# Performance work log

Hardware: AMD Instinct MI355X
Metric: run time of the kernel (lower is better)

The kernel has to match this reference:

```python
import jax, jax.numpy as jnp
import numpy as np

H = 8
LN_EPS = 1e-5

def setup_inputs() -> dict:
    key = jax.random.key(0)
    k1, k2, k3, k4 = jax.random.split(key, 4)
    bh, q_len, dk = 64, 1024, 64
    return {
        "query": jax.random.normal(k1, (bh, q_len, dk), dtype=jnp.float32),
        "key": jax.random.normal(k2, (bh, q_len, dk), dtype=jnp.float32),
        "value": jax.random.normal(k3, (bh, q_len, dk), dtype=jnp.float32),
        "head_att": jax.random.normal(k4, (H, H), dtype=jnp.float32),
        "ln_w": jnp.ones((H,), dtype=jnp.float32),
        "ln_b": jnp.zeros((H,), dtype=jnp.float32),
    }

def reference(query, key, value, head_att, ln_w, ln_b):
    bh, q_len, dk = query.shape
    k_len = key.shape[1]
    # scores: (bh, q, k)
    scores = jnp.einsum("bqd,bkd->bqk", query, key) / jnp.sqrt(jnp.asarray(dk, query.dtype))
    attn = jax.nn.softmax(scores, axis=-1)
    # view as (B, H, q, k) then move heads last: (B, q, k, H)
    a = attn.reshape(-1, H, q_len, k_len).transpose(0, 2, 3, 1)
    # DeepViT re-attention: cross-head mixing matmul
    a = a @ head_att  # (B, q, k, H)
    # LayerNorm over head dim
    mu = a.mean(axis=-1, keepdims=True)
    var = ((a - mu) ** 2).mean(axis=-1, keepdims=True)
    a = (a - mu) * jax.lax.rsqrt(var + LN_EPS) * ln_w + ln_b
    # back to (B, H, q, k)
    a = a.transpose(0, 3, 1, 2)
    att_map = a.mean(axis=1)  # (B, q, k)
    attention = a.reshape(bh, q_len, k_len)
    out = jnp.einsum("bqk,bkd->bqd", attention, value)
    return (out, att_map)
```

## Files before the change

kernel.cpp:

```cpp
#include <hip/hip_runtime.h>
#include <hip/hip_bf16.h>

typedef _Float16 f16;
typedef f16 f16x8 __attribute__((ext_vector_type(8)));
typedef f16 f16x4 __attribute__((ext_vector_type(4)));
typedef float f32x4 __attribute__((ext_vector_type(4)));

#define QL 1024
#define KL 1024
#define DKD 64
#define NH 8
#define LNEPS 1e-5f

__global__ __launch_bounds__(256) void prep_cvt(const float* __restrict__ src,
                                                f16* __restrict__ dst, float scale) {
  int i = (blockIdx.x * 256 + threadIdx.x) * 4;
  float4 v = *reinterpret_cast<const float4*>(src + i);
  f16x4 o;
  o[0] = (f16)(v.x * scale); o[1] = (f16)(v.y * scale);
  o[2] = (f16)(v.z * scale); o[3] = (f16)(v.w * scale);
  *reinterpret_cast<f16x4*>(dst + i) = o;
}

__global__ __launch_bounds__(256) void prep_vt(const float* __restrict__ V, f16* __restrict__ vt) {
  __shared__ float t[32][33];
  const int bh = blockIdx.z, k0 = blockIdx.x * 32, d0 = blockIdx.y * 32;
  const float* src = V + ((size_t)bh * KL + k0) * DKD + d0;
#pragma unroll
  for (int j = 0; j < 4; ++j) {
    int kk = threadIdx.y * 4 + j;
    t[kk][threadIdx.x] = src[kk * DKD + threadIdx.x];
  }
  __syncthreads();
  f16* dst = vt + ((size_t)bh * DKD + d0) * KL + k0;
#pragma unroll
  for (int j = 0; j < 4; ++j) {
    int dd = threadIdx.y * 4 + j;
    dst[dd * KL + threadIdx.x] = (f16)t[threadIdx.x][dd];
  }
}

__global__ __launch_bounds__(256) void stats_kernel(const f16* __restrict__ qf,
    const f16* __restrict__ kf, float* __restrict__ rowsum) {
  const int tid = threadIdx.x;
  const int lane = tid & 63, w = tid >> 6;
  const int m = lane & 15, g = lane >> 4;
  const int id = blockIdx.x;
  const int bh = (id & 7) * 8 + ((id >> 3) & 7);
  const int q0 = (id >> 6) * 64 + w * 16;

  f16x8 qv[2];
#pragma unroll
  for (int dc = 0; dc < 2; ++dc)
    qv[dc] = *reinterpret_cast<const f16x8*>(
        qf + ((size_t)bh * QL + q0 + m) * DKD + dc * 32 + g * 8);

  float part[4] = {0.f, 0.f, 0.f, 0.f};
#pragma unroll 2
  for (int kt = 0; kt < 64; ++kt) {
    const f16* kb = kf + ((size_t)bh * KL + kt * 16 + m) * DKD + g * 8;
    f16x8 k0f = *reinterpret_cast<const f16x8*>(kb);
    f16x8 k1f = *reinterpret_cast<const f16x8*>(kb + 32);
    f32x4 acc = {0.f, 0.f, 0.f, 0.f};
    acc = __builtin_amdgcn_mfma_f32_16x16x32_f16(qv[0], k0f, acc, 0, 0, 0);
    acc = __builtin_amdgcn_mfma_f32_16x16x32_f16(qv[1], k1f, acc, 0, 0, 0);
#pragma unroll
    for (int ri = 0; ri < 4; ++ri) part[ri] += __expf(acc[ri]);
  }
#pragma unroll
  for (int ri = 0; ri < 4; ++ri) {
    float v = part[ri];
    v += __shfl_xor(v, 1); v += __shfl_xor(v, 2);
    v += __shfl_xor(v, 4); v += __shfl_xor(v, 8);
    part[ri] = v;
  }
  if (m == 0) {
#pragma unroll
    for (int ri = 0; ri < 4; ++ri) rowsum[(size_t)bh * QL + q0 + g * 4 + ri] = part[ri];
  }
}

__global__ __launch_bounds__(256) void main_kernel(
    const f16* __restrict__ qf, const f16* __restrict__ kf, const f16* __restrict__ vt,
    const float* __restrict__ rowsum,
    const float* __restrict__ hA, const float* __restrict__ lnw, const float* __restrict__ lnb,
    float* __restrict__ outp, float* __restrict__ part1, float* __restrict__ att_map) {
  __shared__ __align__(16) f16 y_lds[2][NH][16][64];

  const int tid = threadIdx.x;
  const int lane = tid & 63, w = tid >> 6;
  const int m = lane & 15, g = lane >> 4;
  const int id = blockIdx.x;
  const int b = id & 7, kc = (id >> 3) & 1, q0 = (id >> 4) * 16;

  float haR[64], wR[8], bR[8];
#pragma unroll
  for (int j = 0; j < 64; ++j) haR[j] = hA[j];
#pragma unroll
  for (int j = 0; j < 8; ++j) { wR[j] = lnw[j]; bR[j] = lnb[j]; }

  f16x8 qv[NH][2];
#pragma unroll
  for (int h = 0; h < NH; ++h)
#pragma unroll
    for (int dc = 0; dc < 2; ++dc)
      qv[h][dc] = *reinterpret_cast<const f16x8*>(
          qf + (((size_t)(b * NH + h)) * QL + q0 + m) * DKD + dc * 32 + g * 8);

  float inv_rs[NH][4];
#pragma unroll
  for (int h = 0; h < NH; ++h)
#pragma unroll
    for (int ri = 0; ri < 4; ++ri)
      inv_rs[h][ri] = 1.0f / rowsum[(size_t)(b * NH + h) * QL + q0 + g * 4 + ri];

  const size_t kbase_b = (size_t)b * NH * KL;
  f32x4 oacc[2][4];
#pragma unroll
  for (int hp = 0; hp < 2; ++hp)
#pragma unroll
    for (int dt = 0; dt < 4; ++dt) oacc[hp][dt] = (f32x4){0.f, 0.f, 0.f, 0.f};

  for (int kt = 0; kt < 8; ++kt) {
    const int kbase = kc * 512 + kt * 64;
    const int kcol = kbase + w * 16;
    const int buf = kt & 1;

    f32x4 pacc[NH];
    {
      const f16* kb = kf + (kbase_b + kcol + m) * DKD + g * 8;
#pragma unroll
      for (int h = 0; h < NH; ++h) {
        f16x8 k0f = *reinterpret_cast<const f16x8*>(kb + (size_t)h * KL * DKD);
        f16x8 k1f = *reinterpret_cast<const f16x8*>(kb + (size_t)h * KL * DKD + 32);
        f32x4 acc = {0.f, 0.f, 0.f, 0.f};
        acc = __builtin_amdgcn_mfma_f32_16x16x32_f16(qv[h][0], k0f, acc, 0, 0, 0);
        acc = __builtin_amdgcn_mfma_f32_16x16x32_f16(qv[h][1], k1f, acc, 0, 0, 0);
        pacc[h] = acc;
      }
    }
#pragma unroll
    for (int h = 0; h < NH; ++h)
#pragma unroll
      for (int ri = 0; ri < 4; ++ri)
        pacc[h][ri] = __expf(pacc[h][ri]) * inv_rs[h][ri];

#pragma unroll
    for (int ri = 0; ri < 4; ++ri) {
      const int qq = g * 4 + ri;
      float mixed[8];
      float mu = 0.f;
#pragma unroll
      for (int hh = 0; hh < 8; ++hh) {
        float s = 0.f;
#pragma unroll
        for (int j = 0; j < 8; ++j) s = fmaf(pacc[j][ri], haR[j * 8 + hh], s);
        mixed[hh] = s; mu += s;
      }
      mu *= 0.125f;
      float var = 0.f;
#pragma unroll
      for (int hh = 0; hh < 8; ++hh) { float d = mixed[hh] - mu; var = fmaf(d, d, var); }
      var *= 0.125f;
      const float rsv = rsqrtf(var + LNEPS);
      float am = 0.f;
      const int kidx = ((((2 * w + (m >> 3)) ^ (qq & 7)) << 3) | (m & 7));
#pragma unroll
      for (int hh = 0; hh < 8; ++hh) {
        float y = (mixed[hh] - mu) * rsv * wR[hh] + bR[hh];
        am += y;
        y_lds[buf][hh][qq][kidx] = (f16)y;
      }
      att_map[((size_t)b * QL + q0 + qq) * KL + kcol + m] = am * 0.125f;
    }
    __syncthreads();

#pragma unroll
    for (int hp = 0; hp < 2; ++hp) {
      const int hh = w + hp * 4;
      const f16* vb = vt + (((size_t)(b * NH + hh)) * DKD + m) * KL + kbase + g * 8;
#pragma unroll
      for (int ks = 0; ks < 2; ++ks) {
        const f16x8 af = *reinterpret_cast<const f16x8*>(
            &y_lds[buf][hh][m][((ks * 4 + g) ^ (m & 7)) << 3]);
#pragma unroll
        for (int dt = 0; dt < 4; ++dt) {
          f16x8 vf = *reinterpret_cast<const f16x8*>(vb + (size_t)dt * 16 * KL + ks * 32);
          oacc[hp][dt] = __builtin_amdgcn_mfma_f32_16x16x32_f16(af, vf, oacc[hp][dt], 0, 0, 0);
        }
      }
    }
  }

  float* dst = kc ? part1 : outp;
#pragma unroll
  for (int hp = 0; hp < 2; ++hp) {
    const int hh = w + hp * 4;
#pragma unroll
    for (int dt = 0; dt < 4; ++dt)
#pragma unroll
      for (int ri = 0; ri < 4; ++ri)
        dst[(((size_t)(b * NH + hh)) * QL + q0 + g * 4 + ri) * DKD + dt * 16 + m] =
            oacc[hp][dt][ri];
  }
}

__global__ __launch_bounds__(256) void reduce_kernel(const float* __restrict__ p1,
                                                     float* __restrict__ outp) {
  size_t i = ((size_t)blockIdx.x * 256 + threadIdx.x) * 4;
  float4 a = *reinterpret_cast<const float4*>(outp + i);
  float4 c = *reinterpret_cast<const float4*>(p1 + i);
  a.x += c.x; a.y += c.y; a.z += c.z; a.w += c.w;
  *reinterpret_cast<float4*>(outp + i) = a;
}

extern "C" void kernel_launch(void* const* d_in, const int* in_sizes, int n_in,
                              void* d_out, int out_size, void* d_ws, size_t ws_size,
                              hipStream_t stream) {
  const float* Qm  = (const float*)d_in[0];
  const float* Km  = (const float*)d_in[1];
  const float* Vm  = (const float*)d_in[2];
  const float* hA  = (const float*)d_in[3];
  const float* lnw = (const float*)d_in[4];
  const float* lnb = (const float*)d_in[5];
  float* outp = (float*)d_out;
  float* att_map = outp + (size_t)64 * QL * DKD;

  char* ws = (char*)d_ws;
  f16* kfp   = (f16*)ws;
  f16* vtp   = (f16*)(ws + (size_t)8388608);
  f16* qfp   = (f16*)(ws + (size_t)16777216);
  float* rsm = (float*)(ws + (size_t)25165824);
  float* p1  = (float*)(ws + (size_t)25427968);

  prep_cvt<<<4096, 256, 0, stream>>>(Km, kfp, 1.0f);
  prep_cvt<<<4096, 256, 0, stream>>>(Qm, qfp, 0.125f);
  prep_vt<<<dim3(32, 2, 64), dim3(32, 8), 0, stream>>>(Vm, vtp);
  stats_kernel<<<1024, 256, 0, stream>>>(qfp, kfp, rsm);
  main_kernel<<<1024, 256, 0, stream>>>(qfp, kfp, vtp, rsm, hA, lnw, lnb, outp, p1, att_map);
  reduce_kernel<<<4096, 256, 0, stream>>>(p1, outp);
}
```

Baseline: 240.8 us.

## Software-pipeline PV matmul and cut register pressure for higher occupancy

Moves the P·V MFMA for the previous tile so it runs after the next tile's QK MFMAs. This lets the LDS double buffer overlap the softmax/LayerNorm work with the value matmul. To free registers, Q fragments are reloaded from global memory every iteration instead of being held, and the inverse row sums are kept as packed fp16. Launch bounds are raised to request four blocks per CU. The fp16 inverse row sums add a small precision loss, and the Q reloads add extra memory traffic.

```diff
diff --git a/kernel.cpp b/kernel.cpp
--- a/kernel.cpp
+++ b/kernel.cpp
@@ -4,6 +4,7 @@
 typedef _Float16 f16;
 typedef f16 f16x8 __attribute__((ext_vector_type(8)));
 typedef f16 f16x4 __attribute__((ext_vector_type(4)));
+typedef f16 hf2 __attribute__((ext_vector_type(2)));
 typedef float f32x4 __attribute__((ext_vector_type(4)));
 
 #define QL 1024
@@ -80,7 +81,7 @@
   }
 }
 
-__global__ __launch_bounds__(256) void main_kernel(
+__global__ __launch_bounds__(256, 4) void main_kernel(
     const f16* __restrict__ qf, const f16* __restrict__ kf, const f16* __restrict__ vt,
     const float* __restrict__ rowsum,
     const float* __restrict__ hA, const float* __restrict__ lnw, const float* __restrict__ lnb,
@@ -99,28 +100,46 @@
 #pragma unroll
   for (int j = 0; j < 8; ++j) { wR[j] = lnw[j]; bR[j] = lnb[j]; }
 
-  f16x8 qv[NH][2];
+  hf2 irsP[NH][2];
 #pragma unroll
   for (int h = 0; h < NH; ++h)
 #pragma unroll
-    for (int dc = 0; dc < 2; ++dc)
-      qv[h][dc] = *reinterpret_cast<const f16x8*>(
-          qf + (((size_t)(b * NH + h)) * QL + q0 + m) * DKD + dc * 32 + g * 8);
-
-  float inv_rs[NH][4];
-#pragma unroll
-  for (int h = 0; h < NH; ++h)
-#pragma unroll
-    for (int ri = 0; ri < 4; ++ri)
-      inv_rs[h][ri] = 1.0f / rowsum[(size_t)(b * NH + h) * QL + q0 + g * 4 + ri];
-
-  const size_t kbase_b = (size_t)b * NH * KL;
+    for (int rp = 0; rp < 2; ++rp) {
+      const float* rsp = rowsum + (size_t)(b * NH + h) * QL + q0 + g * 4 + 2 * rp;
+      hf2 p;
+      p[0] = (f16)(1.0f / rsp[0]);
+      p[1] = (f16)(1.0f / rsp[1]);
+      irsP[h][rp] = p;
+    }
+
+  const size_t hQ = (size_t)QL * DKD;
+  const f16* qrow = qf + ((size_t)(b * NH) * QL + q0 + m) * DKD + g * 8;
+
   f32x4 oacc[2][4];
 #pragma unroll
   for (int hp = 0; hp < 2; ++hp)
 #pragma unroll
     for (int dt = 0; dt < 4; ++dt) oacc[hp][dt] = (f32x4){0.f, 0.f, 0.f, 0.f};
 
+  auto PV = [&](int bufi, int kb0) {
+#pragma unroll
+    for (int hp = 0; hp < 2; ++hp) {
+      const int hh = w + hp * 4;
+      const f16* vb = vt + (((size_t)(b * NH + hh)) * DKD + m) * KL + kb0 + g * 8;
+#pragma unroll
+      for (int ks = 0; ks < 2; ++ks) {
+        const f16x8 af = *reinterpret_cast<const f16x8*>(
+            &y_lds[bufi][hh][m][((ks * 4 + g) ^ (m & 7)) << 3]);
+#pragma unroll
+        for (int dt = 0; dt < 4; ++dt) {
+          f16x8 vf = *reinterpret_cast<const f16x8*>(vb + (size_t)dt * 16 * KL + ks * 32);
+          oacc[hp][dt] = __builtin_amdgcn_mfma_f32_16x16x32_f16(af, vf, oacc[hp][dt], 0, 0, 0);
+        }
+      }
+    }
+  };
+
+#pragma unroll 2
   for (int kt = 0; kt < 8; ++kt) {
     const int kbase = kc * 512 + kt * 64;
     const int kcol = kbase + w * 16;
@@ -128,22 +147,31 @@
 
     f32x4 pacc[NH];
     {
-      const f16* kb = kf + (kbase_b + kcol + m) * DKD + g * 8;
+      const f16* kb = kf + ((size_t)(b * NH) * KL + kcol + m) * DKD + g * 8;
 #pragma unroll
       for (int h = 0; h < NH; ++h) {
-        f16x8 k0f = *reinterpret_cast<const f16x8*>(kb + (size_t)h * KL * DKD);
-        f16x8 k1f = *reinterpret_cast<const f16x8*>(kb + (size_t)h * KL * DKD + 32);
+        const f16* qp = qrow + h * hQ;
+        f16x8 q0f = *reinterpret_cast<const f16x8*>(qp);
+        f16x8 q1f = *reinterpret_cast<const f16x8*>(qp + 32);
+        const f16* kh = kb + h * (size_t)KL * DKD;
+        f16x8 k0f = *reinterpret_cast<const f16x8*>(kh);
+        f16x8 k1f = *reinterpret_cast<const f16x8*>(kh + 32);
         f32x4 acc = {0.f, 0.f, 0.f, 0.f};
-        acc = __builtin_amdgcn_mfma_f32_16x16x32_f16(qv[h][0], k0f, acc, 0, 0, 0);
-        acc = __builtin_amdgcn_mfma_f32_16x16x32_f16(qv[h][1], k1f, acc, 0, 0, 0);
+        acc = __builtin_amdgcn_mfma_f32_16x16x32_f16(q0f, k0f, acc, 0, 0, 0);
+        acc = __builtin_amdgcn_mfma_f32_16x16x32_f16(q1f, k1f, acc, 0, 0, 0);
         pacc[h] = acc;
       }
     }
-#pragma unroll
-    for (int h = 0; h < NH; ++h)
-#pragma unroll
-      for (int ri = 0; ri < 4; ++ri)
-        pacc[h][ri] = __expf(pacc[h][ri]) * inv_rs[h][ri];
+
+    if (kt) PV(buf ^ 1, kbase - 64);
+
+#pragma unroll
+    for (int h = 0; h < NH; ++h) {
+      pacc[h][0] = __expf(pacc[h][0]) * (float)irsP[h][0][0];
+      pacc[h][1] = __expf(pacc[h][1]) * (float)irsP[h][0][1];
+      pacc[h][2] = __expf(pacc[h][2]) * (float)irsP[h][1][0];
+      pacc[h][3] = __expf(pacc[h][3]) * (float)irsP[h][1][1];
+    }
 
 #pragma unroll
     for (int ri = 0; ri < 4; ++ri) {
@@ -174,23 +202,8 @@
       att_map[((size_t)b * QL + q0 + qq) * KL + kcol + m] = am * 0.125f;
     }
     __syncthreads();
-
-#pragma unroll
-    for (int hp = 0; hp < 2; ++hp) {
-      const int hh = w + hp * 4;
-      const f16* vb = vt + (((size_t)(b * NH + hh)) * DKD + m) * KL + kbase + g * 8;
-#pragma unroll
-      for (int ks = 0; ks < 2; ++ks) {
-        const f16x8 af = *reinterpret_cast<const f16x8*>(
-            &y_lds[buf][hh][m][((ks * 4 + g) ^ (m & 7)) << 3]);
-#pragma unroll
-        for (int dt = 0; dt < 4; ++dt) {
-          f16x8 vf = *reinterpret_cast<const f16x8*>(vb + (size_t)dt * 16 * KL + ks * 32);
-          oacc[hp][dt] = __builtin_amdgcn_mfma_f32_16x16x32_f16(af, vf, oacc[hp][dt], 0, 0, 0);
-        }
-      }
-    }
-  }
+  }
+  PV(1, kc * 512 + 448);
 
   float* dst = kc ? part1 : outp;
 #pragma unroll
```

New measurement: 311.1 us. 1.29x slower.
